# Performance work log

Hardware: AMD Instinct MI355X
Metric: run time of the kernel (lower is better)

## Reference

```python
import jax, jax.numpy as jnp
import numpy as np


def setup_inputs() -> dict:
    key = jax.random.key(0)
    k1, k2, k3, k4, k5 = jax.random.split(key, 5)
    bs, ns, seq_len = 32, 512, 1024
    n_heads, d_r, d_model = 8, 64, 256
    return {
        "x": jax.random.normal(k1, (bs, ns, seq_len), dtype=jnp.float32),
        "routers": jax.random.normal(k2, (n_heads, d_r, d_model), dtype=jnp.float32),
        "w_kv_weight": jax.random.normal(k3, (n_heads * d_model, seq_len), dtype=jnp.float32) * 0.02,
        "proj_weight": jax.random.normal(k4, (seq_len, n_heads * d_model), dtype=jnp.float32) * 0.02,
        "proj_bias": jax.random.normal(k5, (seq_len,), dtype=jnp.float32) * 0.02,
    }


def reference(x, routers, w_kv_weight, proj_weight, proj_bias):
    # x: (bs, ns, seq_len); routers: (H, d_r, d_model)
    bs, ns, _ = x.shape
    H, d_r, d_model = routers.shape
    qk_scale = 1.0 / jnp.sqrt(jnp.asarray(d_model, x.dtype))
    # shared K=V projection: (bs, ns, H*d_model) -> (bs, H, ns, d_model)
    kv = (x @ w_kv_weight.T).reshape(bs, ns, H, d_model).transpose(0, 2, 1, 3)
    # low-rank learned queries attend over the ns axis: (bs, H, d_r, ns)
    attn_score = jnp.einsum('hrd,bhnd->bhrn', routers, kv) * qk_scale
    attn_weight = jax.nn.softmax(attn_score, axis=-1)
    # dropout is identity in eval/reference mode
    out = jnp.einsum('bhrn,bhnd->bhrd', attn_weight, kv)  # (bs, H, d_r, d_model)
    out = out.transpose(0, 2, 1, 3).reshape(bs, d_r, H * d_model)
    out = out @ proj_weight.T + proj_bias  # (bs, d_r, seq_len)
    return out, attn_weight
```

## Files before the change

### kernel.cpp

```cpp
#include <hip/hip_runtime.h>
#include <hip/hip_bf16.h>


typedef __attribute__((ext_vector_type(8))) short short8;
typedef __attribute__((ext_vector_type(4))) short short4v;
typedef __attribute__((ext_vector_type(4))) float f32x4;
typedef __attribute__((ext_vector_type(4))) unsigned int uint4v;
typedef __attribute__((ext_vector_type(4))) unsigned short ushort4v;

__device__ inline unsigned short f2bf(float f) {
  unsigned int u = __float_as_uint(f);
  u += 0x7FFFu + ((u >> 16) & 1u);
  return (unsigned short)(u >> 16);
}

__device__ __forceinline__ void async_copy16(unsigned short* lds, const unsigned short* g) {
  __builtin_amdgcn_global_load_lds(
      (const __attribute__((address_space(1))) unsigned int*)g,
      (__attribute__((address_space(3))) unsigned int*)lds,
      16, 0, 0);
}

__global__ __launch_bounds__(256) void cast_f32_bf16(const float* __restrict__ in,
                                                     unsigned short* __restrict__ out, int n4) {
  int i = blockIdx.x * 256 + threadIdx.x;
  if (i >= n4) return;
  float4 v = ((const float4*)in)[i];
  ushort4v w; w.x = f2bf(v.x); w.y = f2bf(v.y); w.z = f2bf(v.z); w.w = f2bf(v.w);
  ((ushort4v*)out)[i] = w;
}

__global__ __launch_bounds__(512, 1) void gemm1_8phase(
    const unsigned short* __restrict__ A, const unsigned short* __restrict__ B,
    unsigned short* __restrict__ C, int lda, int ldb, int ldc, int K, int nWGn)
{
  __shared__ __align__(16) unsigned short sA[2][2][8192];
  __shared__ __align__(16) unsigned short sB[2][2][8192];

  const int tid = threadIdx.x;
  const int cpx = gridDim.x >> 3;
  const int swz = (blockIdx.x & 7) * cpx + (blockIdx.x >> 3);
  const int bn = swz % nWGn, bm = swz / nWGn;

  const int wave = tid >> 6, lane = tid & 63;
  const int wm = wave >> 2, wn = wave & 3;
  const int lr = lane & 15, ls = lane >> 4;

  const int r0 = tid >> 2, sl0 = tid & 3;
  const unsigned short* gA = A + (long long)(bm * 256 + r0) * lda + sl0 * 8;
  const unsigned short* gB = B + (long long)(bn * 256 + r0) * ldb + sl0 * 8;
  const long long lda128 = (long long)128 * lda, ldb128 = (long long)128 * ldb;

#define STA(b_, k_, t_) { const unsigned short* g_ = gA + (t_) * 64 + (k_) * 32; \
    async_copy16(&sA[b_][k_][tid * 8], g_); \
    async_copy16(&sA[b_][k_][4096 + tid * 8], g_ + lda128); }
#define STB(b_, k_, t_) { const unsigned short* g_ = gB + (t_) * 64 + (k_) * 32; \
    async_copy16(&sB[b_][k_][tid * 8], g_); \
    async_copy16(&sB[b_][k_][4096 + tid * 8], g_ + ldb128); }

  f32x4 acc[8][4];
  #pragma unroll
  for (int mi = 0; mi < 8; ++mi)
    #pragma unroll
    for (int ni = 0; ni < 4; ++ni)
      acc[mi][ni] = f32x4{0.f, 0.f, 0.f, 0.f};

  const int KT = K >> 6;
  STB(0, 0, 0) STA(0, 0, 0) STB(0, 1, 0) STA(0, 1, 0)
  if (KT > 1) {
    STB(1, 0, 1) STA(1, 0, 1) STB(1, 1, 1)
    asm volatile("s_waitcnt vmcnt(6)" ::: "memory");
  } else {
    asm volatile("s_waitcnt vmcnt(0)" ::: "memory");
  }
  __builtin_amdgcn_s_barrier();
  __builtin_amdgcn_sched_barrier(0);

  for (int t = 0; t < KT; ++t) {
    const int b = t & 1, nb = b ^ 1;
    const bool hasT1 = (t + 1) < KT, hasT2 = (t + 2) < KT;
    short8 af[4], bf[4];

    #pragma unroll
    for (int mi = 0; mi < 4; ++mi)
      af[mi] = *(const short8*)&sA[b][0][(wm * 128 + mi * 16 + lr) * 32 + ls * 8];
    #pragma unroll
    for (int ni = 0; ni < 4; ++ni)
      bf[ni] = *(const short8*)&sB[b][0][(wn * 64 + ni * 16 + lr) * 32 + ls * 8];
    if (hasT1) { STA(nb, 1, t + 1) }
    __builtin_amdgcn_s_barrier();
    __builtin_amdgcn_s_setprio(1);
    #pragma unroll
    for (int mi = 0; mi < 4; ++mi)
      #pragma unroll
      for (int ni = 0; ni < 4; ++ni)
        acc[mi][ni] = __builtin_amdgcn_mfma_f32_16x16x32_bf16(af[mi], bf[ni], acc[mi][ni], 0, 0, 0);
    __builtin_amdgcn_s_setprio(0);
    __builtin_amdgcn_s_barrier();

    #pragma unroll
    for (int mi = 0; mi < 4; ++mi)
      af[mi] = *(const short8*)&sA[b][0][(wm * 128 + (4 + mi) * 16 + lr) * 32 + ls * 8];
    if (hasT2) { STB(b, 0, t + 2) }
    __builtin_amdgcn_s_barrier();
    __builtin_amdgcn_s_setprio(1);
    #pragma unroll
    for (int mi = 0; mi < 4; ++mi)
      #pragma unroll
      for (int ni = 0; ni < 4; ++ni)
        acc[4 + mi][ni] = __builtin_amdgcn_mfma_f32_16x16x32_bf16(af[mi], bf[ni], acc[4 + mi][ni], 0, 0, 0);
    __builtin_amdgcn_s_setprio(0);
    __builtin_amdgcn_s_barrier();

    #pragma unroll
    for (int mi = 0; mi < 4; ++mi)
      af[mi] = *(const short8*)&sA[b][1][(wm * 128 + mi * 16 + lr) * 32 + ls * 8];
    #pragma unroll
    for (int ni = 0; ni < 4; ++ni)
      bf[ni] = *(const short8*)&sB[b][1][(wn * 64 + ni * 16 + lr) * 32 + ls * 8];
    if (hasT2) { STA(b, 0, t + 2) }
    __builtin_amdgcn_s_barrier();
    __builtin_amdgcn_s_setprio(1);
    #pragma unroll
    for (int mi = 0; mi < 4; ++mi)
      #pragma unroll
      for (int ni = 0; ni < 4; ++ni)
        acc[mi][ni] = __builtin_amdgcn_mfma_f32_16x16x32_bf16(af[mi], bf[ni], acc[mi][ni], 0, 0, 0);
    __builtin_amdgcn_s_setprio(0);
    __builtin_amdgcn_s_barrier();

    #pragma unroll
    for (int mi = 0; mi < 4; ++mi)
      af[mi] = *(const short8*)&sA[b][1][(wm * 128 + (4 + mi) * 16 + lr) * 32 + ls * 8];
    if (hasT2) { STB(b, 1, t + 2) }
    __builtin_amdgcn_s_barrier();
    __builtin_amdgcn_s_setprio(1);
    #pragma unroll
    for (int mi = 0; mi < 4; ++mi)
      #pragma unroll
      for (int ni = 0; ni < 4; ++ni)
        acc[4 + mi][ni] = __builtin_amdgcn_mfma_f32_16x16x32_bf16(af[mi], bf[ni], acc[4 + mi][ni], 0, 0, 0);
    __builtin_amdgcn_s_setprio(0);
    if (t == KT - 2) {
      asm volatile("s_waitcnt vmcnt(0)" ::: "memory");
    } else if (t < KT - 2) {
      asm volatile("s_waitcnt vmcnt(6)" ::: "memory");
    }
    __builtin_amdgcn_s_barrier();
    __builtin_amdgcn_sched_barrier(0);
  }
#undef STA
#undef STB

  #pragma unroll
  for (int mi = 0; mi < 8; ++mi) {
    #pragma unroll
    for (int ni = 0; ni < 4; ++ni) {
      int row = bm * 256 + wm * 128 + mi * 16 + ls * 4;
      int col = bn * 256 + wn * 64 + ni * 16 + lr;
      #pragma unroll
      for (int r = 0; r < 4; ++r)
        C[(long long)(row + r) * ldc + col] = f2bf(acc[mi][ni][r]);
    }
  }
}

template<int BM,int BN,int BK,int WM,int WN,bool TRANS_B,bool A_F32,bool OUT_BF16,bool DO_SCALE,bool DO_BIAS>
__global__ __launch_bounds__(256) void gemm_bt(
    const void* __restrict__ Av, const unsigned short* __restrict__ Bp,
    void* __restrict__ Cv, const float* __restrict__ bias,
    int lda, int ldb, int ldc, int K, int nWGn,
    long long strAo, long long strAi, long long strBo, long long strBi,
    long long strCo, long long strCi, int binner, float scale)
{
  constexpr int PADA = 8;
  constexpr int PADB = TRANS_B ? 4 : 8;
  constexpr int STRA = BK + PADA;
  constexpr int STRB = BK + PADB;
  constexpr int NWN = BN / WN;
  constexpr int MF = WM / 16, NF = WN / 16;
  __shared__ __align__(16) unsigned short lds_a[BM * STRA];
  __shared__ __align__(16) unsigned short lds_b[BN * STRB];

  const int tid = threadIdx.x;
  const int bn = blockIdx.x % nWGn;
  const int bm = blockIdx.x / nWGn;
  const int batch = blockIdx.y;
  const int bo = batch / binner, bi = batch % binner;

  const int wave = tid >> 6, lane = tid & 63;
  const int wm = wave / NWN, wn = wave % NWN;
  const int lr = lane & 15;
  const int lk = (lane >> 4) * 8;

  const long long abase = bo*strAo + bi*strAi + (long long)bm*BM*lda;
  const long long bbase = bo*strBo + bi*strBi;

  f32x4 acc[MF][NF];
  #pragma unroll
  for (int mi = 0; mi < MF; ++mi)
    #pragma unroll
    for (int ni = 0; ni < NF; ++ni)
      acc[mi][ni] = f32x4{0.f, 0.f, 0.f, 0.f};

  for (int k0 = 0; k0 < K; k0 += BK) {
    if constexpr (A_F32) {
      const float* Af = (const float*)Av + abase + k0;
      #pragma unroll
      for (int i = 0; i < BM*BK/1024; ++i) {
        int c = i*256 + tid;
        int r = c / (BK/4);
        int kc = (c % (BK/4)) * 4;
        float4 v = *(const float4*)(Af + (long long)r*lda + kc);
        ushort4v w; w.x=f2bf(v.x); w.y=f2bf(v.y); w.z=f2bf(v.z); w.w=f2bf(v.w);
        *(ushort4v*)&lds_a[r*STRA + kc] = w;
      }
    } else {
      const unsigned short* Ab2 = (const unsigned short*)Av + abase + k0;
      #pragma unroll
      for (int i = 0; i < BM*BK/2048; ++i) {
        int c = i*256 + tid;
        int r = c / (BK/8);
        int kc = (c % (BK/8)) * 8;
        *(uint4v*)&lds_a[r*STRA + kc] = *(const uint4v*)(Ab2 + (long long)r*lda + kc);
      }
    }
    if constexpr (!TRANS_B) {
      const unsigned short* Bb2 = Bp + bbase + (long long)bn*BN*ldb + k0;
      #pragma unroll
      for (int i = 0; i < BN*BK/2048; ++i) {
        int c = i*256 + tid;
        int r = c / (BK/8);
        int kc = (c % (BK/8)) * 8;
        *(uint4v*)&lds_b[r*STRB + kc] = *(const uint4v*)(Bb2 + (long long)r*ldb + kc);
      }
    } else {
      const unsigned short* Bb2 = Bp + bbase + (long long)k0*ldb + (long long)bn*BN;
      #pragma unroll
      for (int i = 0; i < BN*BK/2048; ++i) {
        int c = i*256 + tid;
        int kr = c / (BN/8);
        int nc = (c % (BN/8)) * 8;
        uint4v v = *(const uint4v*)(Bb2 + (long long)kr*ldb + nc);
        const unsigned short* pv = (const unsigned short*)&v;
        #pragma unroll
        for (int j = 0; j < 8; ++j) lds_b[(nc+j)*STRB + kr] = pv[j];
      }
    }
    __syncthreads();

    #pragma unroll
    for (int kk = 0; kk < BK/32; ++kk) {
      short8 af[MF]; short8 bfr[NF];
      #pragma unroll
      for (int mi = 0; mi < MF; ++mi)
        af[mi] = *(const short8*)&lds_a[(wm*WM + mi*16 + lr)*STRA + kk*32 + lk];
      #pragma unroll
      for (int ni = 0; ni < NF; ++ni) {
        if constexpr (TRANS_B) {
          int base = (wn*WN + ni*16 + lr)*STRB + kk*32 + lk;
          short4v lo = *(const short4v*)&lds_b[base];
          short4v hi = *(const short4v*)&lds_b[base + 4];
          short8 t; t[0]=lo[0]; t[1]=lo[1]; t[2]=lo[2]; t[3]=lo[3];
                    t[4]=hi[0]; t[5]=hi[1]; t[6]=hi[2]; t[7]=hi[3];
          bfr[ni] = t;
        } else {
          bfr[ni] = *(const short8*)&lds_b[(wn*WN + ni*16 + lr)*STRB + kk*32 + lk];
        }
      }
      #pragma unroll
      for (int mi = 0; mi < MF; ++mi)
        #pragma unroll
        for (int ni = 0; ni < NF; ++ni)
          acc[mi][ni] = __builtin_amdgcn_mfma_f32_16x16x32_bf16(af[mi], bfr[ni], acc[mi][ni], 0, 0, 0);
    }
    __syncthreads();
  }

  const long long cbase = bo*strCo + bi*strCi;
  const int cr0 = (lane >> 4) * 4;
  #pragma unroll
  for (int mi = 0; mi < MF; ++mi) {
    #pragma unroll
    for (int ni = 0; ni < NF; ++ni) {
      int row = bm*BM + wm*WM + mi*16 + cr0;
      int col = bn*BN + wn*WN + ni*16 + lr;
      float badd = DO_BIAS ? bias[col] : 0.f;
      #pragma unroll
      for (int r = 0; r < 4; ++r) {
        float x = acc[mi][ni][r];
        if constexpr (DO_SCALE) x *= scale;
        x += badd;
        long long addr = cbase + (long long)(row + r)*ldc + col;
        if constexpr (OUT_BF16) ((unsigned short*)Cv)[addr] = f2bf(x);
        else                    ((float*)Cv)[addr] = x;
      }
    }
  }
}

__global__ __launch_bounds__(256) void softmax_rows(float* __restrict__ sc,
                                                    unsigned short* __restrict__ P) {
  int row = blockIdx.x * 4 + (threadIdx.x >> 6);
  int lane = threadIdx.x & 63;
  float* rp = sc + (long long)row * 512 + lane * 8;
  float4 a = *(const float4*)rp;
  float4 b = *(const float4*)(rp + 4);
  float v[8] = {a.x, a.y, a.z, a.w, b.x, b.y, b.z, b.w};
  float m = v[0];
  #pragma unroll
  for (int i = 1; i < 8; ++i) m = fmaxf(m, v[i]);
  #pragma unroll
  for (int d = 1; d < 64; d <<= 1) m = fmaxf(m, __shfl_xor(m, d, 64));
  float s = 0.f;
  #pragma unroll
  for (int i = 0; i < 8; ++i) { v[i] = __expf(v[i] - m); s += v[i]; }
  #pragma unroll
  for (int d = 1; d < 64; d <<= 1) s += __shfl_xor(s, d, 64);
  float inv = 1.0f / s;
  #pragma unroll
  for (int i = 0; i < 8; ++i) v[i] *= inv;
  float4 oa = {v[0], v[1], v[2], v[3]}, ob = {v[4], v[5], v[6], v[7]};
  *(float4*)rp = oa; *(float4*)(rp + 4) = ob;
  unsigned short* pp = P + (long long)row * 512 + lane * 8;
  ushort4v w0, w1;
  w0.x=f2bf(v[0]); w0.y=f2bf(v[1]); w0.z=f2bf(v[2]); w0.w=f2bf(v[3]);
  w1.x=f2bf(v[4]); w1.y=f2bf(v[5]); w1.z=f2bf(v[6]); w1.w=f2bf(v[7]);
  *(ushort4v*)pp = w0; *(ushort4v*)(pp + 4) = w1;
}

extern "C" void kernel_launch(void* const* d_in, const int* in_sizes, int n_in,
                              void* d_out, int out_size, void* d_ws, size_t ws_size,
                              hipStream_t stream) {
  const float* x       = (const float*)d_in[0];
  const float* routers = (const float*)d_in[1];
  const float* wkv     = (const float*)d_in[2];
  const float* projw   = (const float*)d_in[3];
  const float* pbias   = (const float*)d_in[4];

  char* ws = (char*)d_ws;
  unsigned short* wkv_b   = (unsigned short*)(ws);
  unsigned short* projw_b = (unsigned short*)(ws +  4194304);
  unsigned short* kv_b    = (unsigned short*)(ws +  8388608);
  unsigned short* xb        = (unsigned short*)(ws + 75497472);
  unsigned short* routers_b = (unsigned short*)(ws + 75497472);
  unsigned short* P_b       = (unsigned short*)(ws + 75759616);
  unsigned short* ao_b      = (unsigned short*)(ws + 92536832);

  float* out0  = (float*)d_out;
  float* attnw = out0 + 2097152;

  cast_f32_bf16<<<2048,  256, 0, stream>>>(wkv,   wkv_b,   524288);
  cast_f32_bf16<<<2048,  256, 0, stream>>>(projw, projw_b, 524288);
  cast_f32_bf16<<<16384, 256, 0, stream>>>(x,     xb,      4194304);

  gemm1_8phase<<<512, 512, 0, stream>>>(xb, wkv_b, kv_b, 1024, 1024, 2048, 1024, 8);

  cast_f32_bf16<<<128, 256, 0, stream>>>(routers, routers_b, 32768);

  gemm_bt<64,128,64,64,32,false,false,false,true,false><<<dim3(4,256), 256, 0, stream>>>(
      routers_b, kv_b, attnw, nullptr, 256, 2048, 512, 256, 4,
      0, 16384, 1048576, 256, 262144, 32768, 8, 0.0625f);

  softmax_rows<<<4096, 256, 0, stream>>>(attnw, P_b);

  gemm_bt<64,128,64,64,32,true,false,true,false,false><<<dim3(2,256), 256, 0, stream>>>(
      P_b, kv_b, ao_b, nullptr, 512, 2048, 2048, 512, 2,
      262144, 32768, 1048576, 256, 131072, 256, 8, 1.0f);

  gemm_bt<64,128,64,64,32,false,false,false,false,true><<<dim3(256,1), 256, 0, stream>>>(
      ao_b, projw_b, out0, pbias, 2048, 2048, 1024, 2048, 8,
      0,0, 0,0, 0,0, 1, 1.0f);
}
```

Measured before the change: 192.7 us.

## Fuse score GEMM, softmax and PV GEMM; swizzle LDS in KV GEMM

Replaces the separate scores GEMM, softmax and P·V GEMM launches with one kernel per batch-head that keeps scores and bf16 probabilities in LDS and writes attention weights once. It also XOR-swizzles the LDS layout of the main KV projection GEMM to reduce bank conflicts. The fused kernel removes large global round-trips of the score matrix, but runs only one block per batch-head with uncached direct global loads and a sync-heavy transposed KV staging loop, which may limit throughput.

Measured after the change: 206.8 us. +7.3%, slower.

```diff
diff --git a/kernel.cpp b/kernel.cpp
--- a/kernel.cpp
+++ b/kernel.cpp
@@ -45,8 +45,10 @@
   const int wave = tid >> 6, lane = tid & 63;
   const int wm = wave >> 2, wn = wave & 3;
   const int lr = lane & 15, ls = lane >> 4;
-
-  const int r0 = tid >> 2, sl0 = tid & 3;
+  const int lsw8 = (ls ^ ((lr >> 1) & 3)) * 8;
+
+  const int r0 = tid >> 2;
+  const int sl0 = (tid & 3) ^ ((tid >> 3) & 3);
   const unsigned short* gA = A + (long long)(bm * 256 + r0) * lda + sl0 * 8;
   const unsigned short* gB = B + (long long)(bn * 256 + r0) * ldb + sl0 * 8;
   const long long lda128 = (long long)128 * lda, ldb128 = (long long)128 * ldb;
@@ -83,10 +85,10 @@
 
     #pragma unroll
     for (int mi = 0; mi < 4; ++mi)
-      af[mi] = *(const short8*)&sA[b][0][(wm * 128 + mi * 16 + lr) * 32 + ls * 8];
+      af[mi] = *(const short8*)&sA[b][0][(wm * 128 + mi * 16 + lr) * 32 + lsw8];
     #pragma unroll
     for (int ni = 0; ni < 4; ++ni)
-      bf[ni] = *(const short8*)&sB[b][0][(wn * 64 + ni * 16 + lr) * 32 + ls * 8];
+      bf[ni] = *(const short8*)&sB[b][0][(wn * 64 + ni * 16 + lr) * 32 + lsw8];
     if (hasT1) { STA(nb, 1, t + 1) }
     __builtin_amdgcn_s_barrier();
     __builtin_amdgcn_s_setprio(1);
@@ -100,7 +102,7 @@
 
     #pragma unroll
     for (int mi = 0; mi < 4; ++mi)
-      af[mi] = *(const short8*)&sA[b][0][(wm * 128 + (4 + mi) * 16 + lr) * 32 + ls * 8];
+      af[mi] = *(const short8*)&sA[b][0][(wm * 128 + (4 + mi) * 16 + lr) * 32 + lsw8];
     if (hasT2) { STB(b, 0, t + 2) }
     __builtin_amdgcn_s_barrier();
     __builtin_amdgcn_s_setprio(1);
@@ -114,10 +116,10 @@
 
     #pragma unroll
     for (int mi = 0; mi < 4; ++mi)
-      af[mi] = *(const short8*)&sA[b][1][(wm * 128 + mi * 16 + lr) * 32 + ls * 8];
+      af[mi] = *(const short8*)&sA[b][1][(wm * 128 + mi * 16 + lr) * 32 + lsw8];
     #pragma unroll
     for (int ni = 0; ni < 4; ++ni)
-      bf[ni] = *(const short8*)&sB[b][1][(wn * 64 + ni * 16 + lr) * 32 + ls * 8];
+      bf[ni] = *(const short8*)&sB[b][1][(wn * 64 + ni * 16 + lr) * 32 + lsw8];
     if (hasT2) { STA(b, 0, t + 2) }
     __builtin_amdgcn_s_barrier();
     __builtin_amdgcn_s_setprio(1);
@@ -131,7 +133,7 @@
 
     #pragma unroll
     for (int mi = 0; mi < 4; ++mi)
-      af[mi] = *(const short8*)&sA[b][1][(wm * 128 + (4 + mi) * 16 + lr) * 32 + ls * 8];
+      af[mi] = *(const short8*)&sA[b][1][(wm * 128 + (4 + mi) * 16 + lr) * 32 + lsw8];
     if (hasT2) { STB(b, 1, t + 2) }
     __builtin_amdgcn_s_barrier();
     __builtin_amdgcn_s_setprio(1);
@@ -162,6 +164,113 @@
       for (int r = 0; r < 4; ++r)
         C[(long long)(row + r) * ldc + col] = f2bf(acc[mi][ni][r]);
     }
+  }
+}
+
+__global__ __launch_bounds__(256, 1) void attn_fused(
+    const unsigned short* __restrict__ R,
+    const unsigned short* __restrict__ kv,
+    float* __restrict__ attnw,
+    unsigned short* __restrict__ ao)
+{
+  __shared__ __align__(16) float S_lds[64 * 512];
+  __shared__ __align__(16) unsigned short kvT[16 * 520];
+
+  const int bh = blockIdx.x;
+  const int b = bh >> 3, h = bh & 7;
+  const int tid = threadIdx.x;
+  const int wave = tid >> 6, lane = tid & 63;
+  const int lr = lane & 15, ls = lane >> 4;
+  const int r0 = wave * 16;
+
+  const unsigned short* kvb = kv + (long long)b * 512 * 2048 + h * 256;
+
+  short8 af[8];
+  #pragma unroll
+  for (int kk = 0; kk < 8; ++kk)
+    af[kk] = *(const short8*)&R[h * 16384 + (r0 + lr) * 256 + kk * 32 + ls * 8];
+
+  for (int nt = 0; nt < 32; nt += 2) {
+    short8 bf0[8], bf1[8];
+    #pragma unroll
+    for (int kk = 0; kk < 8; ++kk) {
+      bf0[kk] = *(const short8*)&kvb[(long long)(nt * 16 + lr) * 2048 + kk * 32 + ls * 8];
+      bf1[kk] = *(const short8*)&kvb[(long long)(nt * 16 + 16 + lr) * 2048 + kk * 32 + ls * 8];
+    }
+    f32x4 a0 = f32x4{0.f, 0.f, 0.f, 0.f}, a1 = f32x4{0.f, 0.f, 0.f, 0.f};
+    #pragma unroll
+    for (int kk = 0; kk < 8; ++kk) {
+      a0 = __builtin_amdgcn_mfma_f32_16x16x32_bf16(af[kk], bf0[kk], a0, 0, 0, 0);
+      a1 = __builtin_amdgcn_mfma_f32_16x16x32_bf16(af[kk], bf1[kk], a1, 0, 0, 0);
+    }
+    #pragma unroll
+    for (int j = 0; j < 4; ++j) {
+      S_lds[(r0 + ls * 4 + j) * 512 + nt * 16 + lr]        = a0[j] * 0.0625f;
+      S_lds[(r0 + ls * 4 + j) * 512 + (nt + 1) * 16 + lr]  = a1[j] * 0.0625f;
+    }
+  }
+
+  unsigned short* Ps = (unsigned short*)S_lds;
+  for (int r = 0; r < 16; ++r) {
+    const int row = r0 + r;
+    float* rp = &S_lds[row * 512 + lane * 8];
+    float4 va = *(const float4*)rp;
+    float4 vb = *(const float4*)(rp + 4);
+    float v[8] = {va.x, va.y, va.z, va.w, vb.x, vb.y, vb.z, vb.w};
+    float m = v[0];
+    #pragma unroll
+    for (int i = 1; i < 8; ++i) m = fmaxf(m, v[i]);
+    #pragma unroll
+    for (int d = 1; d < 64; d <<= 1) m = fmaxf(m, __shfl_xor(m, d, 64));
+    float s = 0.f;
+    #pragma unroll
+    for (int i = 0; i < 8; ++i) { v[i] = __expf(v[i] - m); s += v[i]; }
+    #pragma unroll
+    for (int d = 1; d < 64; d <<= 1) s += __shfl_xor(s, d, 64);
+    float inv = 1.0f / s;
+    #pragma unroll
+    for (int i = 0; i < 8; ++i) v[i] *= inv;
+    float* gw = attnw + (long long)bh * 32768 + row * 512 + lane * 8;
+    *(float4*)gw       = float4{v[0], v[1], v[2], v[3]};
+    *(float4*)(gw + 4) = float4{v[4], v[5], v[6], v[7]};
+    ushort4v w0, w1;
+    w0.x = f2bf(v[0]); w0.y = f2bf(v[1]); w0.z = f2bf(v[2]); w0.w = f2bf(v[3]);
+    w1.x = f2bf(v[4]); w1.y = f2bf(v[5]); w1.z = f2bf(v[6]); w1.w = f2bf(v[7]);
+    unsigned short* pp = &Ps[row * 1024 + lane * 8];
+    *(ushort4v*)pp       = w0;
+    *(ushort4v*)(pp + 4) = w1;
+  }
+
+  short8 pf[16];
+  #pragma unroll
+  for (int kc = 0; kc < 16; ++kc)
+    pf[kc] = *(const short8*)&Ps[(r0 + lr) * 1024 + kc * 32 + ls * 8];
+
+  for (int d0 = 0; d0 < 256; d0 += 16) {
+    #pragma unroll
+    for (int i = 0; i < 2; ++i) {
+      int n = i * 256 + tid;
+      #pragma unroll
+      for (int dg = 0; dg < 2; ++dg) {
+        uint4v v = *(const uint4v*)&kvb[(long long)n * 2048 + d0 + dg * 8];
+        const unsigned short* pv = (const unsigned short*)&v;
+        #pragma unroll
+        for (int q = 0; q < 8; ++q) kvT[(dg * 8 + q) * 520 + n] = pv[q];
+      }
+    }
+    __syncthreads();
+    f32x4 c0 = f32x4{0.f, 0.f, 0.f, 0.f};
+    #pragma unroll
+    for (int kc = 0; kc < 16; ++kc) {
+      short8 b0 = *(const short8*)&kvT[lr * 520 + kc * 32 + ls * 8];
+      c0 = __builtin_amdgcn_mfma_f32_16x16x32_bf16(pf[kc], b0, c0, 0, 0, 0);
+    }
+    #pragma unroll
+    for (int q = 0; q < 4; ++q) {
+      int r = r0 + ls * 4 + q;
+      ao[(long long)(b * 64 + r) * 2048 + h * 256 + d0 + lr] = f2bf(c0[q]);
+    }
+    __syncthreads();
   }
 }
 
@@ -299,36 +408,6 @@
   }
 }
 
-__global__ __launch_bounds__(256) void softmax_rows(float* __restrict__ sc,
-                                                    unsigned short* __restrict__ P) {
-  int row = blockIdx.x * 4 + (threadIdx.x >> 6);
-  int lane = threadIdx.x & 63;
-  float* rp = sc + (long long)row * 512 + lane * 8;
-  float4 a = *(const float4*)rp;
-  float4 b = *(const float4*)(rp + 4);
-  float v[8] = {a.x, a.y, a.z, a.w, b.x, b.y, b.z, b.w};
-  float m = v[0];
-  #pragma unroll
-  for (int i = 1; i < 8; ++i) m = fmaxf(m, v[i]);
-  #pragma unroll
-  for (int d = 1; d < 64; d <<= 1) m = fmaxf(m, __shfl_xor(m, d, 64));
-  float s = 0.f;
-  #pragma unroll
-  for (int i = 0; i < 8; ++i) { v[i] = __expf(v[i] - m); s += v[i]; }
-  #pragma unroll
-  for (int d = 1; d < 64; d <<= 1) s += __shfl_xor(s, d, 64);
-  float inv = 1.0f / s;
-  #pragma unroll
-  for (int i = 0; i < 8; ++i) v[i] *= inv;
-  float4 oa = {v[0], v[1], v[2], v[3]}, ob = {v[4], v[5], v[6], v[7]};
-  *(float4*)rp = oa; *(float4*)(rp + 4) = ob;
-  unsigned short* pp = P + (long long)row * 512 + lane * 8;
-  ushort4v w0, w1;
-  w0.x=f2bf(v[0]); w0.y=f2bf(v[1]); w0.z=f2bf(v[2]); w0.w=f2bf(v[3]);
-  w1.x=f2bf(v[4]); w1.y=f2bf(v[5]); w1.z=f2bf(v[6]); w1.w=f2bf(v[7]);
-  *(ushort4v*)pp = w0; *(ushort4v*)(pp + 4) = w1;
-}
-
 extern "C" void kernel_launch(void* const* d_in, const int* in_sizes, int n_in,
                               void* d_out, int out_size, void* d_ws, size_t ws_size,
                               hipStream_t stream) {
@@ -344,7 +423,6 @@
   unsigned short* kv_b    = (unsigned short*)(ws +  8388608);
   unsigned short* xb        = (unsigned short*)(ws + 75497472);
   unsigned short* routers_b = (unsigned short*)(ws + 75497472);
-  unsigned short* P_b       = (unsigned short*)(ws + 75759616);
   unsigned short* ao_b      = (unsigned short*)(ws + 92536832);
 
   float* out0  = (float*)d_out;
@@ -358,15 +436,7 @@
 
   cast_f32_bf16<<<128, 256, 0, stream>>>(routers, routers_b, 32768);
 
-  gemm_bt<64,128,64,64,32,false,false,false,true,false><<<dim3(4,256), 256, 0, stream>>>(
-      routers_b, kv_b, attnw, nullptr, 256, 2048, 512, 256, 4,
-      0, 16384, 1048576, 256, 262144, 32768, 8, 0.0625f);
-
-  softmax_rows<<<4096, 256, 0, stream>>>(attnw, P_b);
-
-  gemm_bt<64,128,64,64,32,true,false,true,false,false><<<dim3(2,256), 256, 0, stream>>>(
-      P_b, kv_b, ao_b, nullptr, 512, 2048, 2048, 512, 2,
-      262144, 32768, 1048576, 256, 131072, 256, 8, 1.0f);
+  attn_fused<<<256, 256, 0, stream>>>(routers_b, kv_b, attnw, ao_b);
 
   gemm_bt<64,128,64,64,32,false,false,false,false,true><<<dim3(256,1), 256, 0, stream>>>(
       ao_b, projw_b, out0, pbias, 2048, 2048, 1024, 2048, 8,
```
